# Kernel tuning notes

Hardware: AMD Instinct MI355X
Metric: run time of the kernel (lower is better)

## Reference

```python
import jax, jax.numpy as jnp
import numpy as np

L_MAX = 6
R = 1
IN_IRREPS  = [(256,0),(128,1),(128,2),(64,3),(64,4),(64,5),(64,6)]
HID_IRREPS = [(64,0),(64,1),(64,2),(32,3),(32,4),(32,5),(32,6)]
N_SCALARS = 64
N_GATES = sum(m for m, l in HID_IRREPS if l > 0)  # 256
PRE_IRREPS = [(N_SCALARS,0),(N_GATES,0)] + [(m,l) for m,l in HID_IRREPS if l > 0]
OUT_IRREPS = [(R,l) for l in range(L_MAX+1)]

def _dim(irr):
    return sum(m*(2*l+1) for m, l in irr)

def _wsize(in_irr, out_irr):
    mul_in = {l: m for m, l in in_irr}
    return sum(mul_in[l]*mo for mo, l in out_irr)

def e3linear(x, wflat, in_irr, out_irr):
    # block-diagonal per-irrep linear with e3nn 1/sqrt(fan_in) normalization
    B = x.shape[0]
    blocks = {}
    off = 0
    for mul, l in in_irr:
        d = mul*(2*l+1)
        blocks[l] = (x[:, off:off+d].reshape(B, mul, 2*l+1), mul)
        off += d
    outs = []
    woff = 0
    for mul_out, l in out_irr:
        xb, mul_in = blocks[l]
        w = wflat[woff:woff+mul_in*mul_out].reshape(mul_in, mul_out)
        woff += mul_in*mul_out
        y = jnp.einsum('bim,io->bom', xb, w) * (1.0/np.sqrt(mul_in))
        outs.append(y.reshape(B, mul_out*(2*l+1)))
    return jnp.concatenate(outs, axis=1)

def gate(z):
    # z = [scalars 64x0e | gates 256x0e | gated l>0 irreps]
    s = jax.nn.silu(z[:, :N_SCALARS])
    g = jax.nn.sigmoid(z[:, N_SCALARS:N_SCALARS+N_GATES])
    x = z[:, N_SCALARS+N_GATES:]
    outs = [s]
    goff = 0
    xoff = 0
    for mul, l in HID_IRREPS:
        if l == 0:
            continue
        m = 2*l+1
        xb = x[:, xoff:xoff+mul*m].reshape(-1, mul, m)
        outs.append((xb * g[:, goff:goff+mul, None]).reshape(-1, mul*m))
        goff += mul
        xoff += mul*m
    return jnp.concatenate(outs, axis=1)

def _forward(v_raw, w1, w2, w3, w4):
    x = gate(e3linear(v_raw, w1, IN_IRREPS, PRE_IRREPS))
    x = gate(e3linear(x, w2, HID_IRREPS, PRE_IRREPS))
    x = gate(e3linear(x, w3, HID_IRREPS, PRE_IRREPS))
    c = e3linear(x, w4, HID_IRREPS, OUT_IRREPS)  # [B, 49]
    B = c.shape[0]
    segs = []
    off = 0
    for l in range(L_MAX+1):
        m = 2*l+1
        seg = c[:, off:off+R*m].reshape(B, R, m).transpose(0, 2, 1)  # (B, m, R)
        segs.append(seg)
        off += R*m
    return jnp.concatenate(segs, axis=1)  # (B, 49, R)

def setup_inputs():
    key = jax.random.key(0)
    ks = jax.random.split(key, 5)
    B = 16384
    return {
        "v_raw": jax.random.normal(ks[0], (B, _dim(IN_IRREPS)), jnp.float32),
        "w1": jax.random.normal(ks[1], (_wsize(IN_IRREPS, PRE_IRREPS),), jnp.float32),
        "w2": jax.random.normal(ks[2], (_wsize(HID_IRREPS, PRE_IRREPS),), jnp.float32),
        "w3": jax.random.normal(ks[3], (_wsize(HID_IRREPS, PRE_IRREPS),), jnp.float32),
        "w4": jax.random.normal(ks[4], (_wsize(HID_IRREPS, OUT_IRREPS),), jnp.float32),
    }

def reference(v_raw, w1, w2, w3, w4):
    return _forward(v_raw, w1, w2, w3, w4)
```

## Files before the change

### kernel.cpp

```cpp
#include <hip/hip_runtime.h>
#include <cstddef>


typedef _Float16 half8 __attribute__((ext_vector_type(8)));
typedef _Float16 half4 __attribute__((ext_vector_type(4)));
typedef float    f32x4 __attribute__((ext_vector_type(4)));
typedef float    fvec4 __attribute__((ext_vector_type(4)));

#define B_ROWS   8
#define IN_DIM   3840
#define OUT_COLS 49

#define OFF_STG0 0
#define OFF_HSA  4224
#define OFF_HSB  5376
#define OFF_G1   6528
#define OFF_G2   8640
#define OFF_G3   10752
#define OFF_SW   12864
#define OFF_H1   21568
#define SMEM_ELTS 26176

#define P2BASE 106496
#define P3BASE 139264

__device__ __forceinline__ void wave_fence() {
  asm volatile("s_waitcnt lgkmcnt(0)" ::: "memory");
}

__global__ __launch_bounds__(256) void prep_weights(
    const float* __restrict__ w1, const float* __restrict__ w2,
    const float* __restrict__ w3, _Float16* __restrict__ packed)
{
  static const int K_[24]    = {256,256,128,128,64,64,64,64,  64,64,64,64,32,32,32,32,
                                64,64,64,64,32,32,32,32};
  static const int N_[24]    = {64,256,64,64,32,32,32,32,  64,256,64,64,32,32,32,32,
                                64,256,64,64,32,32,32,32};
  static const int woff_[24] = {0,16384,81920,90112,98304,100352,102400,104448,
                                0,4096,20480,24576,28672,29696,30720,31744,
                                0,4096,20480,24576,28672,29696,30720,31744};
  static const int poff_[24] = {0,16384,81920,90112,98304,100352,102400,104448,
                                106496,110592,126976,131072,135168,136192,137216,138240,
                                139264,143360,159744,163840,167936,168960,169984,171008};
  const int g = blockIdx.x * 256 + threadIdx.x;
  int bi = 0;
#pragma unroll
  for (int i = 1; i < 24; ++i) if (g * 8 >= poff_[i]) bi = i;
  const float* w = (bi < 8) ? w1 : ((bi < 16) ? w2 : w3);
  const int rel8 = g - poff_[bi] / 8;
  const int lane = rel8 & 63;
  const int fi   = rel8 >> 6;
  const int K = K_[bi], N = N_[bi];
  const int KF = K >> 5;
  const int kf = fi % KF;
  const int mt = fi / KF;
  const int k0 = kf * 32 + (lane >> 4) * 8;
  const int o  = mt * 16 + (lane & 15);
  const float scale = 1.0f / sqrtf((float)K);
  half8 vv;
#pragma unroll
  for (int j = 0; j < 8; ++j)
    vv[j] = (_Float16)(w[woff_[bi] + (size_t)(k0 + j) * N + o] * scale);
  *(half8*)(packed + (size_t)g * 8) = vv;
}

template<int L> struct CP {
  static constexpr int TWOL1 = 2 * L + 1;
  static constexpr int MUL   = (L <= 2) ? 128 : 64;
  static constexpr int N1    = (L <= 2) ? 64  : 32;
  static constexpr int KF1   = MUL / 32;
  static constexpr int KF2   = N1 / 32;
  static constexpr int MT    = N1 / 16;
  static constexpr int AP    = MUL + 8;
  static constexpr int HP    = N1 + 8;
  static constexpr int R     = 8 * TWOL1;
  static constexpr int NQ    = (16 * (MUL / 4)) / 64;
  static constexpr int INOFF = (L==1)?256:(L==2)?640:(L==3)?1280:(L==4)?1728:(L==5)?2304:3008;
  static constexpr int P1    = (L==1)?81920:(L==2)?90112:(L==3)?98304:(L==4)?100352:(L==5)?102400:104448;
  static constexpr int P2R   = (L==1)?20480:(L==2)?24576:(L==3)?28672:(L==4)?29696:(L==5)?30720:31744;
  static constexpr int GO    = (L==1)?0:(L==2)?64:(L==3)?128:(L==4)?160:(L==5)?192:224;
  static constexpr int W4O   = (L==1)?64:(L==2)?128:(L==3)?192:(L==4)?224:(L==5)?256:288;
};

template<int L, int CT>
__device__ __forceinline__ void unit_load(const float* __restrict__ vraw,
                                          int b0, float (&rg)[32])
{
  using P = CP<L>;
  const int lane = threadIdx.x & 63;
#pragma unroll
  for (int v = 0; v < P::NQ; ++v) {
    const int flat = v * 64 + lane;
    const int cc = flat & 15;
    const int iq = flat >> 4;
    const int c  = CT * 16 + cc;
    if (c < P::R) {
      const int b = c / P::TWOL1;
      const int m = c - b * P::TWOL1;
      const float* base = vraw + (size_t)(b0 + b) * IN_DIM + P::INOFF + m
                        + (size_t)(iq * 4) * P::TWOL1;
#pragma unroll
      for (int jj = 0; jj < 4; ++jj) rg[v * 4 + jj] = base[(size_t)jj * P::TWOL1];
    }
  }
}

template<int L, int CT>
__device__ __forceinline__ void unit_stage(const float (&rg)[32], _Float16* SW)
{
  using P = CP<L>;
  const int lane = threadIdx.x & 63;
#pragma unroll
  for (int v = 0; v < P::NQ; ++v) {
    const int flat = v * 64 + lane;
    const int cc = flat & 15;
    const int iq = flat >> 4;
    if (CT * 16 + cc < P::R) {
      half4 h;
#pragma unroll
      for (int jj = 0; jj < 4; ++jj) h[jj] = (_Float16)rg[v * 4 + jj];
      *(half4*)(SW + cc * P::AP + iq * 4) = h;
    }
  }
}

template<int L, int CT>
__device__ __forceinline__ void unit_compute(
    _Float16* SW, _Float16* H1, const _Float16* __restrict__ pk,
    const _Float16* G1, const _Float16* G2, const _Float16* G3,
    const float* __restrict__ w4, float* __restrict__ out, int b0)
{
  using P = CP<L>;
  const int lane = threadIdx.x & 63;
  const int col  = lane & 15;
  const int quad = lane >> 4;
  const int c    = CT * 16 + col;
  const bool vc  = c < P::R;
  const int b    = c / P::TWOL1;
  const int m    = c - b * P::TWOL1;
#pragma unroll
  for (int mt = 0; mt < P::MT; ++mt) {
    f32x4 acc = {0.f, 0.f, 0.f, 0.f};
#pragma unroll
    for (int kf = 0; kf < P::KF1; ++kf) {
      const half8 av = *(const half8*)(pk + P::P1 + (size_t)((mt * P::KF1 + kf) * 64 + lane) * 8);
      const half8 bv = *(const half8*)(SW + col * P::AP + kf * 32 + quad * 8);
      acc = __builtin_amdgcn_mfma_f32_16x16x32_f16(av, bv, acc, 0, 0, 0);
    }
    if (vc) {
      const int o0 = mt * 16 + quad * 4;
      const half4 g4 = *(const half4*)(G1 + b * 264 + P::GO + o0);
      half4 hv;
#pragma unroll
      for (int r = 0; r < 4; ++r) hv[r] = (_Float16)(acc[r] * (float)g4[r]);
      *(half4*)(H1 + col * P::HP + o0) = hv;
    }
  }
  wave_fence();
#pragma unroll
  for (int mt = 0; mt < P::MT; ++mt) {
    f32x4 acc = {0.f, 0.f, 0.f, 0.f};
#pragma unroll
    for (int kf = 0; kf < P::KF2; ++kf) {
      const half8 av = *(const half8*)(pk + P2BASE + P::P2R + (size_t)((mt * P::KF2 + kf) * 64 + lane) * 8);
      const half8 bv = *(const half8*)(H1 + col * P::HP + kf * 32 + quad * 8);
      acc = __builtin_amdgcn_mfma_f32_16x16x32_f16(av, bv, acc, 0, 0, 0);
    }
    if (vc) {
      const int o0 = mt * 16 + quad * 4;
      const half4 g4 = *(const half4*)(G2 + b * 264 + P::GO + o0);
      half4 hv;
#pragma unroll
      for (int r = 0; r < 4; ++r) hv[r] = (_Float16)(acc[r] * (float)g4[r]);
      *(half4*)(SW + col * P::HP + o0) = hv;
    }
  }
  wave_fence();
#pragma unroll
  for (int mt = 0; mt < P::MT; ++mt) {
    f32x4 acc = {0.f, 0.f, 0.f, 0.f};
#pragma unroll
    for (int kf = 0; kf < P::KF2; ++kf) {
      const half8 av = *(const half8*)(pk + P3BASE + P::P2R + (size_t)((mt * P::KF2 + kf) * 64 + lane) * 8);
      const half8 bv = *(const half8*)(SW + col * P::HP + kf * 32 + quad * 8);
      acc = __builtin_amdgcn_mfma_f32_16x16x32_f16(av, bv, acc, 0, 0, 0);
    }
    if (vc) {
      const int o0 = mt * 16 + quad * 4;
      const half4 g4 = *(const half4*)(G3 + b * 264 + P::GO + o0);
      half4 hv;
#pragma unroll
      for (int r = 0; r < 4; ++r) hv[r] = (_Float16)(acc[r] * (float)g4[r]);
      *(half4*)(H1 + col * P::HP + o0) = hv;
    }
  }
  wave_fence();
  float s = 0.f;
  if (vc) {
    constexpr int SEG = P::N1 / 4;
#pragma unroll
    for (int h8 = 0; h8 < SEG / 8; ++h8) {
      const half8 hv = *(const half8*)(H1 + col * P::HP + quad * SEG + h8 * 8);
#pragma unroll
      for (int j = 0; j < 8; ++j)
        s += (float)hv[j] * w4[P::W4O + quad * SEG + h8 * 8 + j];
    }
  }
  s += __shfl_xor(s, 16, 64);
  s += __shfl_xor(s, 32, 64);
  if (vc && quad == 0) {
    constexpr float scale = (P::N1 == 64) ? 0.125f : 0.17677669529663687f;
    out[(size_t)(b0 + b) * OUT_COLS + L * L + m] = s * scale;
  }
}

__device__ __forceinline__ void ws_l0(const fvec4 (&regs)[2], _Float16* stg)
{
  const int t = threadIdx.x;
#pragma unroll
  for (int v = 0; v < 2; ++v) {
    const int gv = v * 256 + t;
    const int b  = gv >> 6;
    const int i0 = (gv & 63) * 4;
    const fvec4 x = regs[v];
    half4 h;
#pragma unroll
    for (int j = 0; j < 4; ++j) h[j] = (_Float16)x[j];
    *(half4*)(stg + b * 264 + i0) = h;
  }
}

template<int K>
__device__ __forceinline__ void scal_sw(
    const _Float16* __restrict__ Bact, const _Float16* __restrict__ ApS,
    const _Float16* __restrict__ ApG, _Float16* __restrict__ HsOut,
    _Float16* __restrict__ Gout, int AP_)
{
  constexpr int KF = K / 32;
  const int lane = threadIdx.x & 63;
  const int wave = threadIdx.x >> 6;
  const int col  = lane & 15;
  const int quad = lane >> 4;
  const _Float16* bp = Bact + col * AP_ + quad * 8;
  {
    const int mt = wave;
    f32x4 acc = {0.f, 0.f, 0.f, 0.f};
    const _Float16* ap = ApS + ((size_t)(mt * KF * 64 + lane)) * 8;
#pragma unroll
    for (int kf = 0; kf < KF; ++kf)
      acc = __builtin_amdgcn_mfma_f32_16x16x32_f16(
          *(const half8*)(ap + kf * 512), *(const half8*)(bp + kf * 32), acc, 0, 0, 0);
    if (col < B_ROWS) {
      const int o0 = mt * 16 + quad * 4;
      half4 hv;
#pragma unroll
      for (int r = 0; r < 4; ++r) {
        const float z = acc[r];
        hv[r] = (_Float16)(z / (1.f + __expf(-z)));
      }
      *(half4*)(HsOut + col * 72 + o0) = hv;
    }
  }
#pragma unroll
  for (int mt0 = 0; mt0 < 4; ++mt0) {
    const int mt = mt0 * 4 + wave;
    f32x4 acc = {0.f, 0.f, 0.f, 0.f};
    const _Float16* ap = ApG + ((size_t)(mt * KF * 64 + lane)) * 8;
#pragma unroll
    for (int kf = 0; kf < KF; ++kf)
      acc = __builtin_amdgcn_mfma_f32_16x16x32_f16(
          *(const half8*)(ap + kf * 512), *(const half8*)(bp + kf * 32), acc, 0, 0, 0);
    if (col < B_ROWS) {
      const int o0 = mt * 16 + quad * 4;
      half4 gv;
#pragma unroll
      for (int r = 0; r < 4; ++r)
        gv[r] = (_Float16)(1.f / (1.f + __expf(-acc[r])));
      *(half4*)(Gout + col * 264 + o0) = gv;
    }
  }
}

__device__ __forceinline__ void scalar_dot(const _Float16* __restrict__ Hs,
                                           const float* __restrict__ w4,
                                           float* __restrict__ out, int b0)
{
  const int r = threadIdx.x;
  if (r < B_ROWS) {
    float s = 0.f;
#pragma unroll
    for (int i8 = 0; i8 < 8; ++i8) {
      const half8 hv = *(const half8*)(Hs + r * 72 + i8 * 8);
#pragma unroll
      for (int j = 0; j < 8; ++j) s += (float)hv[j] * w4[i8 * 8 + j];
    }
    out[(size_t)(b0 + r) * OUT_COLS] = s * 0.125f;
  }
}

__global__ __launch_bounds__(256, 3) void fused_decoder(
    const float* __restrict__ vraw, const float* __restrict__ w4,
    const _Float16* __restrict__ pk, float* __restrict__ out)
{
  __shared__ __align__(16) _Float16 smem[SMEM_ELTS];
  _Float16* STG0 = smem + OFF_STG0;
  _Float16* HsA  = smem + OFF_HSA;
  _Float16* HsB  = smem + OFF_HSB;
  _Float16* G1   = smem + OFF_G1;
  _Float16* G2   = smem + OFF_G2;
  _Float16* G3   = smem + OFF_G3;
  const int wv = threadIdx.x >> 6;
  _Float16* SW = smem + OFF_SW + wv * 2176;
  _Float16* H1 = smem + OFF_H1 + wv * 1152;
  const int b0 = blockIdx.x * B_ROWS;

  fvec4 rA[2];
  {
    const int t = threadIdx.x;
#pragma unroll
    for (int v = 0; v < 2; ++v) {
      const int gv = v * 256 + t;
      rA[v] = *(const fvec4*)(vraw + (size_t)(b0 + (gv >> 6)) * IN_DIM + (gv & 63) * 4);
    }
  }
  float rg[32];
  if      (wv == 0) unit_load<2,0>(vraw, b0, rg);
  else if (wv == 1) unit_load<1,0>(vraw, b0, rg);
  else if (wv == 2) unit_load<6,0>(vraw, b0, rg);
  else              unit_load<5,0>(vraw, b0, rg);

  ws_l0(rA, STG0);
  __syncthreads();
  scal_sw<256>(STG0, pk + 0, pk + 16384, HsA, G1, 264);
  __syncthreads();
  scal_sw<64>(HsA, pk + P2BASE, pk + P2BASE + 4096, HsB, G2, 72);
  __syncthreads();
  scal_sw<64>(HsB, pk + P3BASE, pk + P3BASE + 4096, HsA, G3, 72);
  __syncthreads();

#define RUN_PF(Lc, CTc, Ln, CTn)                                   \
  unit_stage<Lc, CTc>(rg, SW); wave_fence();                       \
  unit_load<Ln, CTn>(vraw, b0, rg);                                \
  unit_compute<Lc, CTc>(SW, H1, pk, G1, G2, G3, w4, out, b0);
#define RUN_LAST(Lc, CTc)                                          \
  unit_stage<Lc, CTc>(rg, SW); wave_fence();                       \
  unit_compute<Lc, CTc>(SW, H1, pk, G1, G2, G3, w4, out, b0);

  if (wv == 0) {
    scalar_dot(HsA, w4, out, b0);
    RUN_PF(2,0, 2,1); RUN_PF(2,1, 2,2); RUN_PF(2,2, 3,3);
    RUN_LAST(3,3);
  } else if (wv == 1) {
    RUN_PF(1,0, 1,1); RUN_PF(1,1, 4,0); RUN_PF(4,0, 4,1);
    RUN_PF(4,1, 4,2); RUN_LAST(4,2);
  } else if (wv == 2) {
    RUN_PF(6,0, 6,1); RUN_PF(6,1, 6,2); RUN_PF(6,2, 6,3);
    RUN_PF(6,3, 6,4); RUN_PF(6,4, 6,5); RUN_PF(6,5, 6,6);
    RUN_PF(6,6, 3,0); RUN_PF(3,0, 3,1); RUN_LAST(3,1);
  } else {
    RUN_PF(5,0, 5,1); RUN_PF(5,1, 5,2); RUN_PF(5,2, 5,3);
    RUN_PF(5,3, 5,4); RUN_PF(5,4, 5,5); RUN_PF(5,5, 4,3);
    RUN_PF(4,3, 4,4); RUN_PF(4,4, 3,2); RUN_LAST(3,2);
  }
#undef RUN_PF
#undef RUN_LAST
}

extern "C" void kernel_launch(void* const* d_in, const int* in_sizes, int n_in,
                              void* d_out, int out_size, void* d_ws, size_t ws_size,
                              hipStream_t stream)
{
  (void)in_sizes; (void)n_in; (void)out_size; (void)ws_size;
  const float* vraw = (const float*)d_in[0];
  const float* w1   = (const float*)d_in[1];
  const float* w2   = (const float*)d_in[2];
  const float* w3   = (const float*)d_in[3];
  const float* w4   = (const float*)d_in[4];
  float* out = (float*)d_out;
  _Float16* packed = (_Float16*)d_ws;

  prep_weights<<<84, 256, 0, stream>>>(w1, w2, w3, packed);
  fused_decoder<<<16384 / B_ROWS, 256, 0, stream>>>(vraw, w4, packed, out);
}
```

Baseline: 431.5 us.

## Process 16 rows per block with register-resident MFMA fragments and rebalanced wave chains

Doubles the batch rows per block to 16 so every MFMA column is a valid row, removing masked lanes and the padded staging buffer. Input fragments are now loaded straight into registers in MFMA layout rather than staged through shared memory, and the last gated layer is fused with the w4 dot product so one LDS round trip disappears. The per-wave work split across irreps is rebalanced using templated chains with double-buffered prefetch. Fewer blocks per CU (launch bounds 2) and higher register use may reduce occupancy.

New measurement: 374.9 us. -13.1%, faster.

```diff
diff --git a/kernel.cpp b/kernel.cpp
--- a/kernel.cpp
+++ b/kernel.cpp
@@ -7,26 +7,22 @@
 typedef float    f32x4 __attribute__((ext_vector_type(4)));
 typedef float    fvec4 __attribute__((ext_vector_type(4)));
 
-#define B_ROWS   8
+#define B_ROWS   16
 #define IN_DIM   3840
 #define OUT_COLS 49
-
-#define OFF_STG0 0
-#define OFF_HSA  4224
-#define OFF_HSB  5376
-#define OFF_G1   6528
-#define OFF_G2   8640
-#define OFF_G3   10752
-#define OFF_SW   12864
-#define OFF_H1   21568
-#define SMEM_ELTS 26176
+#define GP  264
+#define HSP 72
+
+#define OFF_G1  0
+#define OFF_G2  4224
+#define OFF_G3  8448
+#define OFF_HS1 12672
+#define OFF_HS2 13824
+#define OFF_SCR 14976
+#define SMEM_ELTS 24192
 
 #define P2BASE 106496
 #define P3BASE 139264
-
-__device__ __forceinline__ void wave_fence() {
-  asm volatile("s_waitcnt lgkmcnt(0)" ::: "memory");
-}
 
 __global__ __launch_bounds__(256) void prep_weights(
     const float* __restrict__ w1, const float* __restrict__ w2,
@@ -66,304 +62,312 @@
 
 template<int L> struct CP {
   static constexpr int TWOL1 = 2 * L + 1;
-  static constexpr int MUL   = (L <= 2) ? 128 : 64;
-  static constexpr int N1    = (L <= 2) ? 64  : 32;
-  static constexpr int KF1   = MUL / 32;
-  static constexpr int KF2   = N1 / 32;
-  static constexpr int MT    = N1 / 16;
-  static constexpr int AP    = MUL + 8;
-  static constexpr int HP    = N1 + 8;
-  static constexpr int R     = 8 * TWOL1;
-  static constexpr int NQ    = (16 * (MUL / 4)) / 64;
+  static constexpr int K1  = (L <= 2) ? 128 : 64;
+  static constexpr int N1  = (L <= 2) ? 64  : 32;
+  static constexpr int KF1 = K1 / 32;
+  static constexpr int KF2 = N1 / 32;
+  static constexpr int MT  = N1 / 16;
   static constexpr int INOFF = (L==1)?256:(L==2)?640:(L==3)?1280:(L==4)?1728:(L==5)?2304:3008;
   static constexpr int P1    = (L==1)?81920:(L==2)?90112:(L==3)?98304:(L==4)?100352:(L==5)?102400:104448;
   static constexpr int P2R   = (L==1)?20480:(L==2)?24576:(L==3)?28672:(L==4)?29696:(L==5)?30720:31744;
   static constexpr int GO    = (L==1)?0:(L==2)?64:(L==3)?128:(L==4)?160:(L==5)?192:224;
   static constexpr int W4O   = (L==1)?64:(L==2)?128:(L==3)?192:(L==4)?224:(L==5)?256:288;
+  static constexpr float SCALE = (N1 == 64) ? 0.125f : 0.17677669529663687f;
 };
 
-template<int L, int CT>
+template<int L>
 __device__ __forceinline__ void unit_load(const float* __restrict__ vraw,
-                                          int b0, float (&rg)[32])
+                                          int b0, int ct, float (&rg)[CP<L>::KF1 * 8])
 {
   using P = CP<L>;
   const int lane = threadIdx.x & 63;
-#pragma unroll
-  for (int v = 0; v < P::NQ; ++v) {
-    const int flat = v * 64 + lane;
-    const int cc = flat & 15;
-    const int iq = flat >> 4;
-    const int c  = CT * 16 + cc;
-    if (c < P::R) {
-      const int b = c / P::TWOL1;
-      const int m = c - b * P::TWOL1;
-      const float* base = vraw + (size_t)(b0 + b) * IN_DIM + P::INOFF + m
-                        + (size_t)(iq * 4) * P::TWOL1;
-#pragma unroll
-      for (int jj = 0; jj < 4; ++jj) rg[v * 4 + jj] = base[(size_t)jj * P::TWOL1];
-    }
-  }
-}
-
-template<int L, int CT>
-__device__ __forceinline__ void unit_stage(const float (&rg)[32], _Float16* SW)
+  const int col  = lane & 15;
+  const int quad = lane >> 4;
+  const int c = ct * 16 + col;
+  const int b = c / P::TWOL1;
+  const int m = c - b * P::TWOL1;
+  const float* base = vraw + (size_t)(b0 + b) * IN_DIM + P::INOFF + m
+                    + (size_t)(quad * 8) * P::TWOL1;
+#pragma unroll
+  for (int kf = 0; kf < P::KF1; ++kf)
+#pragma unroll
+    for (int j = 0; j < 8; ++j)
+      rg[kf * 8 + j] = base[(size_t)(kf * 32 + j) * P::TWOL1];
+}
+
+template<int L>
+__device__ __forceinline__ void unit_compute(
+    const float (&rg)[CP<L>::KF1 * 8], const _Float16* __restrict__ pk,
+    const _Float16* G1, const _Float16* G2, const _Float16* G3,
+    _Float16* HSa, _Float16* HSb,
+    const float* __restrict__ w4, float* __restrict__ out, int b0, int ct)
 {
   using P = CP<L>;
   const int lane = threadIdx.x & 63;
-#pragma unroll
-  for (int v = 0; v < P::NQ; ++v) {
-    const int flat = v * 64 + lane;
-    const int cc = flat & 15;
-    const int iq = flat >> 4;
-    if (CT * 16 + cc < P::R) {
-      half4 h;
-#pragma unroll
-      for (int jj = 0; jj < 4; ++jj) h[jj] = (_Float16)rg[v * 4 + jj];
-      *(half4*)(SW + cc * P::AP + iq * 4) = h;
-    }
-  }
-}
-
-template<int L, int CT>
-__device__ __forceinline__ void unit_compute(
-    _Float16* SW, _Float16* H1, const _Float16* __restrict__ pk,
-    const _Float16* G1, const _Float16* G2, const _Float16* G3,
-    const float* __restrict__ w4, float* __restrict__ out, int b0)
-{
-  using P = CP<L>;
-  const int lane = threadIdx.x & 63;
-  const int col  = lane & 15;
-  const int quad = lane >> 4;
-  const int c    = CT * 16 + col;
-  const bool vc  = c < P::R;
-  const int b    = c / P::TWOL1;
-  const int m    = c - b * P::TWOL1;
+  const int col  = lane & 15;
+  const int quad = lane >> 4;
+  const int c = ct * 16 + col;
+  const int b = c / P::TWOL1;
+  const int m = c - b * P::TWOL1;
+  half8 bf[P::KF1];
+#pragma unroll
+  for (int kf = 0; kf < P::KF1; ++kf)
+#pragma unroll
+    for (int j = 0; j < 8; ++j) bf[kf][j] = (_Float16)rg[kf * 8 + j];
 #pragma unroll
   for (int mt = 0; mt < P::MT; ++mt) {
     f32x4 acc = {0.f, 0.f, 0.f, 0.f};
 #pragma unroll
     for (int kf = 0; kf < P::KF1; ++kf) {
       const half8 av = *(const half8*)(pk + P::P1 + (size_t)((mt * P::KF1 + kf) * 64 + lane) * 8);
-      const half8 bv = *(const half8*)(SW + col * P::AP + kf * 32 + quad * 8);
-      acc = __builtin_amdgcn_mfma_f32_16x16x32_f16(av, bv, acc, 0, 0, 0);
-    }
-    if (vc) {
-      const int o0 = mt * 16 + quad * 4;
-      const half4 g4 = *(const half4*)(G1 + b * 264 + P::GO + o0);
-      half4 hv;
-#pragma unroll
-      for (int r = 0; r < 4; ++r) hv[r] = (_Float16)(acc[r] * (float)g4[r]);
-      *(half4*)(H1 + col * P::HP + o0) = hv;
-    }
-  }
-  wave_fence();
+      acc = __builtin_amdgcn_mfma_f32_16x16x32_f16(av, bf[kf], acc, 0, 0, 0);
+    }
+    const int o0 = mt * 16 + quad * 4;
+    const half4 g4 = *(const half4*)(G1 + b * GP + P::GO + o0);
+    half4 h;
+#pragma unroll
+    for (int r = 0; r < 4; ++r) h[r] = (_Float16)(acc[r] * (float)g4[r]);
+    *(half4*)(HSa + col * HSP + o0) = h;
+  }
 #pragma unroll
   for (int mt = 0; mt < P::MT; ++mt) {
     f32x4 acc = {0.f, 0.f, 0.f, 0.f};
 #pragma unroll
     for (int kf = 0; kf < P::KF2; ++kf) {
       const half8 av = *(const half8*)(pk + P2BASE + P::P2R + (size_t)((mt * P::KF2 + kf) * 64 + lane) * 8);
-      const half8 bv = *(const half8*)(H1 + col * P::HP + kf * 32 + quad * 8);
+      const half8 bv = *(const half8*)(HSa + col * HSP + kf * 32 + quad * 8);
       acc = __builtin_amdgcn_mfma_f32_16x16x32_f16(av, bv, acc, 0, 0, 0);
     }
-    if (vc) {
-      const int o0 = mt * 16 + quad * 4;
-      const half4 g4 = *(const half4*)(G2 + b * 264 + P::GO + o0);
-      half4 hv;
-#pragma unroll
-      for (int r = 0; r < 4; ++r) hv[r] = (_Float16)(acc[r] * (float)g4[r]);
-      *(half4*)(SW + col * P::HP + o0) = hv;
-    }
-  }
-  wave_fence();
+    const int o0 = mt * 16 + quad * 4;
+    const half4 g4 = *(const half4*)(G2 + b * GP + P::GO + o0);
+    half4 h;
+#pragma unroll
+    for (int r = 0; r < 4; ++r) h[r] = (_Float16)(acc[r] * (float)g4[r]);
+    *(half4*)(HSb + col * HSP + o0) = h;
+  }
+  float s = 0.f;
 #pragma unroll
   for (int mt = 0; mt < P::MT; ++mt) {
     f32x4 acc = {0.f, 0.f, 0.f, 0.f};
 #pragma unroll
     for (int kf = 0; kf < P::KF2; ++kf) {
       const half8 av = *(const half8*)(pk + P3BASE + P::P2R + (size_t)((mt * P::KF2 + kf) * 64 + lane) * 8);
-      const half8 bv = *(const half8*)(SW + col * P::HP + kf * 32 + quad * 8);
+      const half8 bv = *(const half8*)(HSb + col * HSP + kf * 32 + quad * 8);
       acc = __builtin_amdgcn_mfma_f32_16x16x32_f16(av, bv, acc, 0, 0, 0);
     }
-    if (vc) {
-      const int o0 = mt * 16 + quad * 4;
-      const half4 g4 = *(const half4*)(G3 + b * 264 + P::GO + o0);
-      half4 hv;
-#pragma unroll
-      for (int r = 0; r < 4; ++r) hv[r] = (_Float16)(acc[r] * (float)g4[r]);
-      *(half4*)(H1 + col * P::HP + o0) = hv;
-    }
-  }
-  wave_fence();
-  float s = 0.f;
-  if (vc) {
-    constexpr int SEG = P::N1 / 4;
-#pragma unroll
-    for (int h8 = 0; h8 < SEG / 8; ++h8) {
-      const half8 hv = *(const half8*)(H1 + col * P::HP + quad * SEG + h8 * 8);
-#pragma unroll
-      for (int j = 0; j < 8; ++j)
-        s += (float)hv[j] * w4[P::W4O + quad * SEG + h8 * 8 + j];
-    }
+    const int o0 = mt * 16 + quad * 4;
+    const half4 g4 = *(const half4*)(G3 + b * GP + P::GO + o0);
+#pragma unroll
+    for (int r = 0; r < 4; ++r)
+      s += acc[r] * (float)g4[r] * w4[P::W4O + o0 + r];
   }
   s += __shfl_xor(s, 16, 64);
   s += __shfl_xor(s, 32, 64);
-  if (vc && quad == 0) {
-    constexpr float scale = (P::N1 == 64) ? 0.125f : 0.17677669529663687f;
-    out[(size_t)(b0 + b) * OUT_COLS + L * L + m] = s * scale;
-  }
-}
-
-__device__ __forceinline__ void ws_l0(const fvec4 (&regs)[2], _Float16* stg)
-{
-  const int t = threadIdx.x;
-#pragma unroll
-  for (int v = 0; v < 2; ++v) {
-    const int gv = v * 256 + t;
-    const int b  = gv >> 6;
-    const int i0 = (gv & 63) * 4;
-    const fvec4 x = regs[v];
+  if (quad == 0)
+    out[(size_t)(b0 + b) * OUT_COLS + L * L + m] = s * P::SCALE;
+}
+
+template<int L, int CT0, int NCT>
+__device__ __forceinline__ void run_chain(
+    const float* __restrict__ vraw, const _Float16* __restrict__ pk,
+    const _Float16* G1, const _Float16* G2, const _Float16* G3,
+    _Float16* HSa, _Float16* HSb,
+    const float* __restrict__ w4, float* __restrict__ out, int b0)
+{
+  float rg[2][CP<L>::KF1 * 8];
+  unit_load<L>(vraw, b0, CT0, rg[0]);
+#pragma unroll
+  for (int u = 0; u < NCT; ++u) {
+    if (u + 1 < NCT) unit_load<L>(vraw, b0, CT0 + u + 1, rg[(u + 1) & 1]);
+    unit_compute<L>(rg[u & 1], pk, G1, G2, G3, HSa, HSb, w4, out, b0, CT0 + u);
+  }
+}
+
+__device__ __forceinline__ void load_scal_frags(const float* __restrict__ vraw,
+                                                int b0, half8 (&sf)[8])
+{
+  const int lane = threadIdx.x & 63;
+  const int col  = lane & 15;
+  const int quad = lane >> 4;
+  const float* base = vraw + (size_t)(b0 + col) * IN_DIM + quad * 8;
+#pragma unroll
+  for (int kf = 0; kf < 8; ++kf) {
+    const fvec4 a = *(const fvec4*)(base + kf * 32);
+    const fvec4 b2 = *(const fvec4*)(base + kf * 32 + 4);
+#pragma unroll
+    for (int j = 0; j < 4; ++j) { sf[kf][j] = (_Float16)a[j]; sf[kf][4 + j] = (_Float16)b2[j]; }
+  }
+}
+
+__device__ __forceinline__ void scal_L1(const half8 (&sf)[8],
+    const _Float16* __restrict__ pk, _Float16* Hs1, _Float16* G1v)
+{
+  const int lane = threadIdx.x & 63;
+  const int wv   = threadIdx.x >> 6;
+  const int col  = lane & 15;
+  const int quad = lane >> 4;
+  {
+    f32x4 acc = {0.f, 0.f, 0.f, 0.f};
+#pragma unroll
+    for (int kf = 0; kf < 8; ++kf) {
+      const half8 av = *(const half8*)(pk + (size_t)((wv * 8 + kf) * 64 + lane) * 8);
+      acc = __builtin_amdgcn_mfma_f32_16x16x32_f16(av, sf[kf], acc, 0, 0, 0);
+    }
+    const int o0 = wv * 16 + quad * 4;
     half4 h;
 #pragma unroll
-    for (int j = 0; j < 4; ++j) h[j] = (_Float16)x[j];
-    *(half4*)(stg + b * 264 + i0) = h;
-  }
-}
-
-template<int K>
-__device__ __forceinline__ void scal_sw(
-    const _Float16* __restrict__ Bact, const _Float16* __restrict__ ApS,
-    const _Float16* __restrict__ ApG, _Float16* __restrict__ HsOut,
-    _Float16* __restrict__ Gout, int AP_)
-{
-  constexpr int KF = K / 32;
-  const int lane = threadIdx.x & 63;
-  const int wave = threadIdx.x >> 6;
-  const int col  = lane & 15;
-  const int quad = lane >> 4;
-  const _Float16* bp = Bact + col * AP_ + quad * 8;
+    for (int r = 0; r < 4; ++r) { const float z = acc[r]; h[r] = (_Float16)(z / (1.f + __expf(-z))); }
+    *(half4*)(Hs1 + col * HSP + o0) = h;
+  }
+#pragma unroll
+  for (int t = 0; t < 4; ++t) {
+    const int mt = wv * 4 + t;
+    f32x4 acc = {0.f, 0.f, 0.f, 0.f};
+#pragma unroll
+    for (int kf = 0; kf < 8; ++kf) {
+      const half8 av = *(const half8*)(pk + 16384 + (size_t)((mt * 8 + kf) * 64 + lane) * 8);
+      acc = __builtin_amdgcn_mfma_f32_16x16x32_f16(av, sf[kf], acc, 0, 0, 0);
+    }
+    const int o0 = mt * 16 + quad * 4;
+    half4 g;
+#pragma unroll
+    for (int r = 0; r < 4; ++r) g[r] = (_Float16)(1.f / (1.f + __expf(-acc[r])));
+    *(half4*)(G1v + col * GP + o0) = g;
+  }
+}
+
+__device__ __forceinline__ void scal_mid(const _Float16* HsIn,
+    const _Float16* __restrict__ pkS, const _Float16* __restrict__ pkG,
+    _Float16* HsOut, _Float16* Gv)
+{
+  const int lane = threadIdx.x & 63;
+  const int wv   = threadIdx.x >> 6;
+  const int col  = lane & 15;
+  const int quad = lane >> 4;
+  half8 bf[2];
+#pragma unroll
+  for (int kf = 0; kf < 2; ++kf)
+    bf[kf] = *(const half8*)(HsIn + col * HSP + kf * 32 + quad * 8);
   {
-    const int mt = wave;
-    f32x4 acc = {0.f, 0.f, 0.f, 0.f};
-    const _Float16* ap = ApS + ((size_t)(mt * KF * 64 + lane)) * 8;
-#pragma unroll
-    for (int kf = 0; kf < KF; ++kf)
-      acc = __builtin_amdgcn_mfma_f32_16x16x32_f16(
-          *(const half8*)(ap + kf * 512), *(const half8*)(bp + kf * 32), acc, 0, 0, 0);
-    if (col < B_ROWS) {
+    f32x4 acc = {0.f, 0.f, 0.f, 0.f};
+#pragma unroll
+    for (int kf = 0; kf < 2; ++kf) {
+      const half8 av = *(const half8*)(pkS + (size_t)((wv * 2 + kf) * 64 + lane) * 8);
+      acc = __builtin_amdgcn_mfma_f32_16x16x32_f16(av, bf[kf], acc, 0, 0, 0);
+    }
+    const int o0 = wv * 16 + quad * 4;
+    half4 h;
+#pragma unroll
+    for (int r = 0; r < 4; ++r) { const float z = acc[r]; h[r] = (_Float16)(z / (1.f + __expf(-z))); }
+    *(half4*)(HsOut + col * HSP + o0) = h;
+  }
+#pragma unroll
+  for (int t = 0; t < 4; ++t) {
+    const int mt = wv * 4 + t;
+    f32x4 acc = {0.f, 0.f, 0.f, 0.f};
+#pragma unroll
+    for (int kf = 0; kf < 2; ++kf) {
+      const half8 av = *(const half8*)(pkG + (size_t)((mt * 2 + kf) * 64 + lane) * 8);
+      acc = __builtin_amdgcn_mfma_f32_16x16x32_f16(av, bf[kf], acc, 0, 0, 0);
+    }
+    const int o0 = mt * 16 + quad * 4;
+    half4 g;
+#pragma unroll
+    for (int r = 0; r < 4; ++r) g[r] = (_Float16)(1.f / (1.f + __expf(-acc[r])));
+    *(half4*)(Gv + col * GP + o0) = g;
+  }
+}
+
+__device__ __forceinline__ void scal_last(const _Float16* Hs2,
+    const _Float16* __restrict__ pkS, const _Float16* __restrict__ pkG,
+    _Float16* G3v, const float* __restrict__ w4, float* __restrict__ out, int b0)
+{
+  const int lane = threadIdx.x & 63;
+  const int wv   = threadIdx.x >> 6;
+  const int col  = lane & 15;
+  const int quad = lane >> 4;
+  half8 bf[2];
+#pragma unroll
+  for (int kf = 0; kf < 2; ++kf)
+    bf[kf] = *(const half8*)(Hs2 + col * HSP + kf * 32 + quad * 8);
+  if (wv == 0) {
+    float s = 0.f;
+#pragma unroll
+    for (int mt = 0; mt < 4; ++mt) {
+      f32x4 acc = {0.f, 0.f, 0.f, 0.f};
+#pragma unroll
+      for (int kf = 0; kf < 2; ++kf) {
+        const half8 av = *(const half8*)(pkS + (size_t)((mt * 2 + kf) * 64 + lane) * 8);
+        acc = __builtin_amdgcn_mfma_f32_16x16x32_f16(av, bf[kf], acc, 0, 0, 0);
+      }
       const int o0 = mt * 16 + quad * 4;
-      half4 hv;
 #pragma unroll
       for (int r = 0; r < 4; ++r) {
         const float z = acc[r];
-        hv[r] = (_Float16)(z / (1.f + __expf(-z)));
+        s += (z / (1.f + __expf(-z))) * w4[o0 + r];
       }
-      *(half4*)(HsOut + col * 72 + o0) = hv;
-    }
-  }
-#pragma unroll
-  for (int mt0 = 0; mt0 < 4; ++mt0) {
-    const int mt = mt0 * 4 + wave;
-    f32x4 acc = {0.f, 0.f, 0.f, 0.f};
-    const _Float16* ap = ApG + ((size_t)(mt * KF * 64 + lane)) * 8;
-#pragma unroll
-    for (int kf = 0; kf < KF; ++kf)
-      acc = __builtin_amdgcn_mfma_f32_16x16x32_f16(
-          *(const half8*)(ap + kf * 512), *(const half8*)(bp + kf * 32), acc, 0, 0, 0);
-    if (col < B_ROWS) {
+    }
+    s += __shfl_xor(s, 16, 64);
+    s += __shfl_xor(s, 32, 64);
+    if (quad == 0) out[(size_t)(b0 + col) * OUT_COLS] = s * 0.125f;
+  } else {
+    const int t0 = (wv == 1) ? 0 : (wv == 2) ? 6 : 11;
+    const int tn = (wv == 1) ? 6 : 5;
+    for (int t = 0; t < tn; ++t) {
+      const int mt = t0 + t;
+      f32x4 acc = {0.f, 0.f, 0.f, 0.f};
+#pragma unroll
+      for (int kf = 0; kf < 2; ++kf) {
+        const half8 av = *(const half8*)(pkG + (size_t)((mt * 2 + kf) * 64 + lane) * 8);
+        acc = __builtin_amdgcn_mfma_f32_16x16x32_f16(av, bf[kf], acc, 0, 0, 0);
+      }
       const int o0 = mt * 16 + quad * 4;
-      half4 gv;
-#pragma unroll
-      for (int r = 0; r < 4; ++r)
-        gv[r] = (_Float16)(1.f / (1.f + __expf(-acc[r])));
-      *(half4*)(Gout + col * 264 + o0) = gv;
-    }
-  }
-}
-
-__device__ __forceinline__ void scalar_dot(const _Float16* __restrict__ Hs,
-                                           const float* __restrict__ w4,
-                                           float* __restrict__ out, int b0)
-{
-  const int r = threadIdx.x;
-  if (r < B_ROWS) {
-    float s = 0.f;
-#pragma unroll
-    for (int i8 = 0; i8 < 8; ++i8) {
-      const half8 hv = *(const half8*)(Hs + r * 72 + i8 * 8);
-#pragma unroll
-      for (int j = 0; j < 8; ++j) s += (float)hv[j] * w4[i8 * 8 + j];
-    }
-    out[(size_t)(b0 + r) * OUT_COLS] = s * 0.125f;
-  }
-}
-
-__global__ __launch_bounds__(256, 3) void fused_decoder(
+      half4 g;
+#pragma unroll
+      for (int r = 0; r < 4; ++r) g[r] = (_Float16)(1.f / (1.f + __expf(-acc[r])));
+      *(half4*)(G3v + col * GP + o0) = g;
+    }
+  }
+}
+
+__global__ __launch_bounds__(256, 2) void fused_decoder(
     const float* __restrict__ vraw, const float* __restrict__ w4,
     const _Float16* __restrict__ pk, float* __restrict__ out)
 {
   __shared__ __align__(16) _Float16 smem[SMEM_ELTS];
-  _Float16* STG0 = smem + OFF_STG0;
-  _Float16* HsA  = smem + OFF_HSA;
-  _Float16* HsB  = smem + OFF_HSB;
-  _Float16* G1   = smem + OFF_G1;
-  _Float16* G2   = smem + OFF_G2;
-  _Float16* G3   = smem + OFF_G3;
+  _Float16* G1  = smem + OFF_G1;
+  _Float16* G2  = smem + OFF_G2;
+  _Float16* G3  = smem + OFF_G3;
+  _Float16* Hs1 = smem + OFF_HS1;
+  _Float16* Hs2 = smem + OFF_HS2;
   const int wv = threadIdx.x >> 6;
-  _Float16* SW = smem + OFF_SW + wv * 2176;
-  _Float16* H1 = smem + OFF_H1 + wv * 1152;
+  _Float16* HSa = smem + OFF_SCR + wv * 2304;
+  _Float16* HSb = HSa + 1152;
   const int b0 = blockIdx.x * B_ROWS;
 
-  fvec4 rA[2];
-  {
-    const int t = threadIdx.x;
-#pragma unroll
-    for (int v = 0; v < 2; ++v) {
-      const int gv = v * 256 + t;
-      rA[v] = *(const fvec4*)(vraw + (size_t)(b0 + (gv >> 6)) * IN_DIM + (gv & 63) * 4);
-    }
-  }
-  float rg[32];
-  if      (wv == 0) unit_load<2,0>(vraw, b0, rg);
-  else if (wv == 1) unit_load<1,0>(vraw, b0, rg);
-  else if (wv == 2) unit_load<6,0>(vraw, b0, rg);
-  else              unit_load<5,0>(vraw, b0, rg);
-
-  ws_l0(rA, STG0);
+  half8 sf[8];
+  load_scal_frags(vraw, b0, sf);
+  scal_L1(sf, pk, Hs1, G1);
   __syncthreads();
-  scal_sw<256>(STG0, pk + 0, pk + 16384, HsA, G1, 264);
+  scal_mid(Hs1, pk + P2BASE, pk + P2BASE + 4096, Hs2, G2);
   __syncthreads();
-  scal_sw<64>(HsA, pk + P2BASE, pk + P2BASE + 4096, HsB, G2, 72);
+  scal_last(Hs2, pk + P3BASE, pk + P3BASE + 4096, G3, w4, out, b0);
   __syncthreads();
-  scal_sw<64>(HsB, pk + P3BASE, pk + P3BASE + 4096, HsA, G3, 72);
-  __syncthreads();
-
-#define RUN_PF(Lc, CTc, Ln, CTn)                                   \
-  unit_stage<Lc, CTc>(rg, SW); wave_fence();                       \
-  unit_load<Ln, CTn>(vraw, b0, rg);                                \
-  unit_compute<Lc, CTc>(SW, H1, pk, G1, G2, G3, w4, out, b0);
-#define RUN_LAST(Lc, CTc)                                          \
-  unit_stage<Lc, CTc>(rg, SW); wave_fence();                       \
-  unit_compute<Lc, CTc>(SW, H1, pk, G1, G2, G3, w4, out, b0);
 
   if (wv == 0) {
-    scalar_dot(HsA, w4, out, b0);
-    RUN_PF(2,0, 2,1); RUN_PF(2,1, 2,2); RUN_PF(2,2, 3,3);
-    RUN_LAST(3,3);
+    run_chain<2, 0, 5>(vraw, pk, G1, G2, G3, HSa, HSb, w4, out, b0);
+    run_chain<3, 0, 4>(vraw, pk, G1, G2, G3, HSa, HSb, w4, out, b0);
   } else if (wv == 1) {
-    RUN_PF(1,0, 1,1); RUN_PF(1,1, 4,0); RUN_PF(4,0, 4,1);
-    RUN_PF(4,1, 4,2); RUN_LAST(4,2);
+    run_chain<1, 0, 3>(vraw, pk, G1, G2, G3, HSa, HSb, w4, out, b0);
+    run_chain<3, 4, 3>(vraw, pk, G1, G2, G3, HSa, HSb, w4, out, b0);
+    run_chain<4, 0, 5>(vraw, pk, G1, G2, G3, HSa, HSb, w4, out, b0);
   } else if (wv == 2) {
-    RUN_PF(6,0, 6,1); RUN_PF(6,1, 6,2); RUN_PF(6,2, 6,3);
-    RUN_PF(6,3, 6,4); RUN_PF(6,4, 6,5); RUN_PF(6,5, 6,6);
-    RUN_PF(6,6, 3,0); RUN_PF(3,0, 3,1); RUN_LAST(3,1);
+    run_chain<6, 0, 13>(vraw, pk, G1, G2, G3, HSa, HSb, w4, out, b0);
+    run_chain<4, 5, 1>(vraw, pk, G1, G2, G3, HSa, HSb, w4, out, b0);
   } else {
-    RUN_PF(5,0, 5,1); RUN_PF(5,1, 5,2); RUN_PF(5,2, 5,3);
-    RUN_PF(5,3, 5,4); RUN_PF(5,4, 5,5); RUN_PF(5,5, 4,3);
-    RUN_PF(4,3, 4,4); RUN_PF(4,4, 3,2); RUN_LAST(3,2);
-  }
-#undef RUN_PF
-#undef RUN_LAST
+    run_chain<5, 0, 11>(vraw, pk, G1, G2, G3, HSa, HSb, w4, out, b0);
+    run_chain<4, 6, 3>(vraw, pk, G1, G2, G3, HSa, HSb, w4, out, b0);
+  }
 }
 
 extern "C" void kernel_launch(void* const* d_in, const int* in_sizes, int n_in,
```
